# Optimization experiments

Hardware: AMD Instinct MI355X
Metric: run time of the kernel (lower is better)

The kernel has to match this reference:

```python
import jax, jax.numpy as jnp
import numpy as np
import math

HIDDEN = 1024
HEADS = 16
D_K = HIDDEN // HEADS
D_FF = 4 * HIDDEN
EPS = 1e-5


def gelu_tanh(x):
    # exact match of the module's hand-written GELU
    c = math.sqrt(2.0 / math.pi)
    return 0.5 * x * (1.0 + jnp.tanh(c * (x + 0.044715 * x ** 3)))


def layer_norm(x, gamma, beta):
    mu = jnp.mean(x, axis=-1, keepdims=True)
    var = jnp.mean((x - mu) ** 2, axis=-1, keepdims=True)
    return (x - mu) * jax.lax.rsqrt(var + EPS) * gamma + beta


def setup_inputs() -> dict:
    key = jax.random.key(0)
    ks = jax.random.split(key, 16)
    s = 0.02
    B, S, H = 4, 2048, HIDDEN
    return {
        "x": jax.random.normal(ks[0], (B, S, H), dtype=jnp.float32),
        "Wq": jax.random.normal(ks[1], (H, H), dtype=jnp.float32) * s,
        "bq": jnp.zeros((H,), jnp.float32),
        "Wk": jax.random.normal(ks[2], (H, H), dtype=jnp.float32) * s,
        "bk": jnp.zeros((H,), jnp.float32),
        "Wv": jax.random.normal(ks[3], (H, H), dtype=jnp.float32) * s,
        "bv": jnp.zeros((H,), jnp.float32),
        "Wo": jax.random.normal(ks[4], (H, H), dtype=jnp.float32) * s,
        "bo": jnp.zeros((H,), jnp.float32),
        "W1": jax.random.normal(ks[5], (H, D_FF), dtype=jnp.float32) * s,
        "b1": jnp.zeros((D_FF,), jnp.float32),
        "W2": jax.random.normal(ks[6], (D_FF, H), dtype=jnp.float32) * s,
        "b2": jnp.zeros((H,), jnp.float32),
        "g1": jnp.ones((H,), jnp.float32),
        "be1": jnp.zeros((H,), jnp.float32),
        "g2": jnp.ones((H,), jnp.float32),
        "be2": jnp.zeros((H,), jnp.float32),
    }


def reference(x, Wq, bq, Wk, bk, Wv, bv, Wo, bo, W1, b1, W2, b2, g1, be1, g2, be2):
    B, S, H = x.shape
    # QKV projections -> [B, heads, S, d_k]
    def split_heads(t):
        return t.reshape(B, S, HEADS, D_K).transpose(0, 2, 1, 3)
    q = split_heads(x @ Wq + bq)
    k = split_heads(x @ Wk + bk)
    v = split_heads(x @ Wv + bv)
    scores = jnp.einsum("bhsd,bhtd->bhst", q, k) / math.sqrt(D_K)
    attn = jax.nn.softmax(scores, axis=-1)
    ctx = jnp.einsum("bhst,bhtd->bhsd", attn, v)
    ctx = ctx.transpose(0, 2, 1, 3).reshape(B, S, H)
    attn_out = ctx @ Wo + bo
    x = layer_norm(x + attn_out, g1, be1)
    ff = gelu_tanh(x @ W1 + b1) @ W2 + b2
    x = layer_norm(x + ff, g2, be2)
    return x
```

## Files before the change

### kernel.cpp

```cpp
#include <hip/hip_runtime.h>
#include <hip/hip_bf16.h>
#include <math.h>

#define HIDDEN 1024
#define NHEADS 16
#define DK 64
#define DFF 4096
#define SEQ 2048
#define NBATCH 4
#define NTOK (NBATCH*SEQ)

typedef __attribute__((ext_vector_type(8))) short bf16x8;
typedef __attribute__((ext_vector_type(4))) float f32x4;
typedef __attribute__((ext_vector_type(16))) float f32x16;
typedef __attribute__((ext_vector_type(4))) unsigned short us4;
typedef __attribute__((ext_vector_type(2))) unsigned int u32x2;

typedef __attribute__((address_space(1))) void gvoid;
typedef __attribute__((address_space(3))) void lvoid;

__device__ __forceinline__ unsigned short f2b(float f) {
  union { float f; unsigned int u; } v; v.f = f;
  unsigned int u = v.u;
  return (unsigned short)((u + 0x7fffu + ((u >> 16) & 1u)) >> 16);
}

__device__ __forceinline__ unsigned pack_bf16(float lo, float hi) {
  float2 f2; f2.x = lo; f2.y = hi;
  __hip_bfloat162 h = __float22bfloat162_rn(f2);
  union { __hip_bfloat162 h; unsigned u; } c; c.h = h;
  return c.u;
}

__device__ __forceinline__ void gload_lds16(const void* g, void* l) {
  __builtin_amdgcn_global_load_lds((gvoid*)g, (lvoid*)l, 16, 0, 0);
}

__global__ void k_cvt(const float* __restrict__ in, unsigned short* __restrict__ out, int n4) {
  int i = blockIdx.x * blockDim.x + threadIdx.x;
  int stride = gridDim.x * blockDim.x;
  for (; i < n4; i += stride) {
    float4 v = ((const float4*)in)[i];
    us4 o;
    o.x = f2b(v.x); o.y = f2b(v.y); o.z = f2b(v.z); o.w = f2b(v.w);
    ((us4*)out)[i] = o;
  }
}

__global__ void k_transcvt(const float* __restrict__ W, unsigned short* __restrict__ WT,
                           int K, int N, float scale) {
  __shared__ unsigned short tile[64][80];
  int t = threadIdx.x;
  int k0 = blockIdx.x * 64, n0 = blockIdx.y * 64;
  int lr = t >> 2, c0 = (t & 3) * 16;
  const float* src = W + (size_t)(k0 + lr) * N + n0 + c0;
  #pragma unroll
  for (int j = 0; j < 16; ++j) tile[lr][c0 + j] = f2b(src[j] * scale);
  __syncthreads();
  unsigned short* dst = WT + (size_t)(n0 + lr) * K + k0 + c0;
  #pragma unroll
  for (int j = 0; j < 16; ++j) dst[j] = tile[c0 + j][lr];
}

__global__ void k_vtrans(const unsigned short* __restrict__ V, unsigned short* __restrict__ VT) {
  __shared__ unsigned short tile[64][80];
  int bid = blockIdx.x;
  int st = bid & 31, bh = bid >> 5;
  int s0 = st * 64;
  int t = threadIdx.x;
  int lr = t >> 2, c0 = (t & 3) * 16;
  const unsigned short* src = V + (size_t)bh * SEQ * DK + (size_t)(s0 + lr) * DK + c0;
  #pragma unroll
  for (int j = 0; j < 16; ++j) tile[lr][c0 + j] = src[j];
  __syncthreads();
  unsigned short* dst = VT + (size_t)bh * DK * SEQ + (size_t)lr * SEQ + s0 + c0;
  #pragma unroll
  for (int j = 0; j < 16; ++j) dst[j] = tile[c0 + j][lr];
}

template <int MODE>
__global__ __launch_bounds__(256)
void k_gemm(const unsigned short* __restrict__ A, const unsigned short* __restrict__ Bt,
            const float* __restrict__ bias, void* __restrict__ Cout,
            int M, int N, int K, float bscale) {
  __shared__ __align__(1024) char lds[32768];
  const int tid = threadIdx.x;
  const int lane = tid & 63;
  const int wid = tid >> 6;
  const int wm = wid >> 1, wn = wid & 1;
  const int l15 = lane & 15, lg = lane >> 4;
  const int bm = blockIdx.x, bn = blockIdx.y;

  f32x4 acc[4][4] = {};

  const char* Ab = (const char*)A + (size_t)bm * 128 * (size_t)K * 2;
  const char* Bb = (const char*)Bt + (size_t)bn * 128 * (size_t)K * 2;
  const size_t ldr = (size_t)K * 2;

  for (int k0 = 0; k0 < K; k0 += 64) {
    #pragma unroll
    for (int r = 0; r < 4; ++r) {
      int li = tid * 16 + r * 4096;
      int row = li >> 7;
      int col = (li & 127) ^ ((row & 7) << 4);
      gload_lds16(Ab + (size_t)row * ldr + k0 * 2 + col, lds + li);
      gload_lds16(Bb + (size_t)row * ldr + k0 * 2 + col, lds + 16384 + li);
    }
    __syncthreads();
    #pragma unroll
    for (int kc = 0; kc < 2; ++kc) {
      bf16x8 af[4], bfr[4];
      #pragma unroll
      for (int i = 0; i < 4; ++i) {
        int kb = kc * 64 + (lg << 4);
        int lr = wm * 64 + i * 16 + l15;
        af[i] = *(const bf16x8*)(lds + lr * 128 + (kb ^ ((lr & 7) << 4)));
        int lr2 = wn * 64 + i * 16 + l15;
        bfr[i] = *(const bf16x8*)(lds + 16384 + lr2 * 128 + (kb ^ ((lr2 & 7) << 4)));
      }
      #pragma unroll
      for (int mi = 0; mi < 4; ++mi)
        #pragma unroll
        for (int ni = 0; ni < 4; ++ni)
          acc[mi][ni] = __builtin_amdgcn_mfma_f32_16x16x32_bf16(af[mi], bfr[ni], acc[mi][ni], 0, 0, 0);
    }
    __syncthreads();
  }

  const int mbase = bm * 128 + wm * 64;
  const int nbase = bn * 128 + wn * 64;
  #pragma unroll
  for (int ni = 0; ni < 4; ++ni) {
    int n = nbase + ni * 16 + l15;
    float bv = bias[n] * bscale;
    #pragma unroll
    for (int mi = 0; mi < 4; ++mi) {
      #pragma unroll
      for (int r = 0; r < 4; ++r) {
        int m = mbase + mi * 16 + lg * 4 + r;
        float val = acc[mi][ni][r] + bv;
        if (MODE == 0) {
          int b = m >> 11, s = m & 2047;
          int h = n >> 6, d = n & 63;
          ((unsigned short*)Cout)[((size_t)(b * NHEADS + h) * SEQ + s) * DK + d] = f2b(val);
        } else if (MODE == 1) {
          ((float*)Cout)[(size_t)m * N + n] = val;
        } else {
          float x = val;
          float t = tanhf(0.7978845608028654f * (x + 0.044715f * x * x * x));
          ((unsigned short*)Cout)[(size_t)m * N + n] = f2b(0.5f * x * (1.0f + t));
        }
      }
    }
  }
}

__global__ __launch_bounds__(256)
void k_attn(const unsigned short* __restrict__ Qp, const unsigned short* __restrict__ Kp,
            const unsigned short* __restrict__ VTp, unsigned short* __restrict__ ctx) {
  const int tid = threadIdx.x, w = tid >> 6, lane = tid & 63;
  const int l31 = lane & 31, hi = lane >> 5;
  const int bid = blockIdx.x;
  const int qb = bid & 15, bh = bid >> 4;
  const size_t base = (size_t)bh * SEQ * DK;
  const size_t baseT = (size_t)bh * DK * SEQ;
  const int q0 = qb * 128 + w * 32;

  const float L2E = 1.4426950408889634f;
  const float THR = 11.541560327111708f;

  bf16x8 qf[4];
  #pragma unroll
  for (int sl = 0; sl < 4; ++sl)
    qf[sl] = *(const bf16x8*)(Qp + base + (size_t)(q0 + l31) * DK + sl * 16 + hi * 8);

  bf16x8 kf[4];
  #pragma unroll
  for (int sl = 0; sl < 4; ++sl)
    kf[sl] = *(const bf16x8*)(Kp + base + (size_t)l31 * DK + sl * 16 + hi * 8);

  float M = -1e30f, l_run = 0.f;
  f32x16 o0 = {}, o1 = {};

  for (int kv0 = 0; kv0 < SEQ; kv0 += 32) {
    f32x16 s = {};
    __builtin_amdgcn_s_setprio(1);
    #pragma unroll
    for (int sl = 0; sl < 4; ++sl)
      s = __builtin_amdgcn_mfma_f32_32x32x16_bf16(kf[sl], qf[sl], s, 0, 0, 0);
    __builtin_amdgcn_s_setprio(0);

    int kvn = kv0 + 32;
    if (kvn < SEQ) {
      #pragma unroll
      for (int sl = 0; sl < 4; ++sl)
        kf[sl] = *(const bf16x8*)(Kp + base + (size_t)(kvn + l31) * DK + sl * 16 + hi * 8);
    }
    bf16x8 vf00 = *(const bf16x8*)(VTp + baseT + (size_t)(l31) * SEQ + kv0 + hi * 8);
    bf16x8 vf01 = *(const bf16x8*)(VTp + baseT + (size_t)(l31) * SEQ + kv0 + 16 + hi * 8);
    bf16x8 vf10 = *(const bf16x8*)(VTp + baseT + (size_t)(32 + l31) * SEQ + kv0 + hi * 8);
    bf16x8 vf11 = *(const bf16x8*)(VTp + baseT + (size_t)(32 + l31) * SEQ + kv0 + 16 + hi * 8);

    float mx = fmaxf(s[0], s[1]);
    #pragma unroll
    for (int r = 2; r < 16; ++r) mx = fmaxf(mx, s[r]);
    mx = fmaxf(mx, __shfl_xor(mx, 32));
    float mxl = mx * L2E;
    if (!__all(mxl <= M + THR)) {
      float Mnew = fmaxf(M, mxl);
      float corr = __builtin_amdgcn_exp2f(M - Mnew);
      l_run *= corr;
      #pragma unroll
      for (int r = 0; r < 16; ++r) { o0[r] *= corr; o1[r] *= corr; }
      M = Mnew;
    }
    float p[16];
    float sum = 0.f;
    #pragma unroll
    for (int r = 0; r < 16; ++r) {
      p[r] = __builtin_amdgcn_exp2f(fmaf(s[r], L2E, -M));
      sum += p[r];
    }
    sum += __shfl_xor(sum, 32);
    l_run += sum;

    unsigned wds[8];
    #pragma unroll
    for (int g = 0; g < 2; ++g) {
      unsigned w0 = pack_bf16(p[g*8+0], p[g*8+1]);
      unsigned w1 = pack_bf16(p[g*8+2], p[g*8+3]);
      unsigned w2 = pack_bf16(p[g*8+4], p[g*8+5]);
      unsigned w3 = pack_bf16(p[g*8+6], p[g*8+7]);
#if __has_builtin(__builtin_amdgcn_permlane32_swap)
      u32x2 r02 = __builtin_amdgcn_permlane32_swap(w0, w2, false, false);
      u32x2 r13 = __builtin_amdgcn_permlane32_swap(w1, w3, false, false);
      wds[g*4+0] = r02.x; wds[g*4+1] = r13.x;
      wds[g*4+2] = r02.y; wds[g*4+3] = r13.y;
#else
      unsigned s0 = __shfl_xor(w0, 32), s1 = __shfl_xor(w1, 32);
      unsigned s2 = __shfl_xor(w2, 32), s3 = __shfl_xor(w3, 32);
      wds[g*4+0] = hi ? s2 : w0; wds[g*4+1] = hi ? s3 : w1;
      wds[g*4+2] = hi ? w2 : s0; wds[g*4+3] = hi ? w3 : s1;
#endif
    }
    union { unsigned u[4]; bf16x8 v; } pb0, pb1;
    pb0.u[0]=wds[0]; pb0.u[1]=wds[1]; pb0.u[2]=wds[2]; pb0.u[3]=wds[3];
    pb1.u[0]=wds[4]; pb1.u[1]=wds[5]; pb1.u[2]=wds[6]; pb1.u[3]=wds[7];

    __builtin_amdgcn_s_setprio(1);
    o0 = __builtin_amdgcn_mfma_f32_32x32x16_bf16(vf00, pb0.v, o0, 0, 0, 0);
    o1 = __builtin_amdgcn_mfma_f32_32x32x16_bf16(vf10, pb0.v, o1, 0, 0, 0);
    o0 = __builtin_amdgcn_mfma_f32_32x32x16_bf16(vf01, pb1.v, o0, 0, 0, 0);
    o1 = __builtin_amdgcn_mfma_f32_32x32x16_bf16(vf11, pb1.v, o1, 0, 0, 0);
    __builtin_amdgcn_s_setprio(0);
  }

  float inv = 1.f / l_run;
  const int b = bh >> 4, h = bh & 15;
  const int q = q0 + l31;
  size_t rowbase = ((size_t)(b * SEQ + q)) * HIDDEN + h * 64;
  #pragma unroll
  for (int g = 0; g < 4; ++g) {
    us4 st0, st1;
    st0.x = f2b(o0[4*g+0] * inv); st0.y = f2b(o0[4*g+1] * inv);
    st0.z = f2b(o0[4*g+2] * inv); st0.w = f2b(o0[4*g+3] * inv);
    st1.x = f2b(o1[4*g+0] * inv); st1.y = f2b(o1[4*g+1] * inv);
    st1.z = f2b(o1[4*g+2] * inv); st1.w = f2b(o1[4*g+3] * inv);
    int d0 = g * 8 + hi * 4;
    *(us4*)(ctx + rowbase + d0)      = st0;
    *(us4*)(ctx + rowbase + 32 + d0) = st1;
  }
}

__global__ __launch_bounds__(256)
void k_ln(const float* __restrict__ a, const float* __restrict__ b,
          const float* __restrict__ gamma, const float* __restrict__ beta,
          float* __restrict__ outf, unsigned short* __restrict__ outb) {
  int row = blockIdx.x;
  int tid = threadIdx.x;
  const float4* A = (const float4*)(a + (size_t)row * HIDDEN);
  const float4* B = (const float4*)(b + (size_t)row * HIDDEN);
  float4 va = A[tid], vb = B[tid];
  float x0 = va.x + vb.x, x1 = va.y + vb.y, x2 = va.z + vb.z, x3 = va.w + vb.w;
  float sum = x0 + x1 + x2 + x3;
  float sq = x0 * x0 + x1 * x1 + x2 * x2 + x3 * x3;
  #pragma unroll
  for (int d = 1; d < 64; d <<= 1) { sum += __shfl_xor(sum, d); sq += __shfl_xor(sq, d); }
  __shared__ float red[8];
  if ((tid & 63) == 0) { red[(tid >> 6) * 2] = sum; red[(tid >> 6) * 2 + 1] = sq; }
  __syncthreads();
  sum = red[0] + red[2] + red[4] + red[6];
  sq  = red[1] + red[3] + red[5] + red[7];
  float mu = sum * (1.f / HIDDEN);
  float var = sq * (1.f / HIDDEN) - mu * mu;
  float rs = rsqrtf(var + 1e-5f);
  float4 g = ((const float4*)gamma)[tid];
  float4 be = ((const float4*)beta)[tid];
  float y0 = (x0 - mu) * rs * g.x + be.x;
  float y1 = (x1 - mu) * rs * g.y + be.y;
  float y2 = (x2 - mu) * rs * g.z + be.z;
  float y3 = (x3 - mu) * rs * g.w + be.w;
  if (outf) { float4 o; o.x = y0; o.y = y1; o.z = y2; o.w = y3; ((float4*)(outf + (size_t)row * HIDDEN))[tid] = o; }
  if (outb) { us4 o; o.x = f2b(y0); o.y = f2b(y1); o.z = f2b(y2); o.w = f2b(y3); ((us4*)(outb + (size_t)row * HIDDEN))[tid] = o; }
}

#define OFF_XB   ((size_t)0)
#define OFF_WQT  ((size_t)16777216)
#define OFF_WKT  ((size_t)18874368)
#define OFF_WVT  ((size_t)20971520)
#define OFF_WOT  ((size_t)23068672)
#define OFF_W1T  ((size_t)25165824)
#define OFF_W2T  ((size_t)33554432)
#define OFF_Q    ((size_t)41943040)
#define OFF_K    ((size_t)58720256)
#define OFF_V    ((size_t)75497472)
#define OFF_VT   ((size_t)92274688)
#define OFF_AO   ((size_t)109051904)
#define OFF_LN1F ((size_t)142606336)

extern "C" void kernel_launch(void* const* d_in, const int* in_sizes, int n_in,
                              void* d_out, int out_size, void* d_ws, size_t ws_size,
                              hipStream_t stream) {
  const float* x   = (const float*)d_in[0];
  const float* Wq  = (const float*)d_in[1];
  const float* bq  = (const float*)d_in[2];
  const float* Wk  = (const float*)d_in[3];
  const float* bk  = (const float*)d_in[4];
  const float* Wv  = (const float*)d_in[5];
  const float* bv  = (const float*)d_in[6];
  const float* Wo  = (const float*)d_in[7];
  const float* bo  = (const float*)d_in[8];
  const float* W1  = (const float*)d_in[9];
  const float* b1  = (const float*)d_in[10];
  const float* W2  = (const float*)d_in[11];
  const float* b2  = (const float*)d_in[12];
  const float* g1  = (const float*)d_in[13];
  const float* be1 = (const float*)d_in[14];
  const float* g2  = (const float*)d_in[15];
  const float* be2 = (const float*)d_in[16];

  char* ws = (char*)d_ws;
  unsigned short* xb   = (unsigned short*)(ws + OFF_XB);
  unsigned short* wqT  = (unsigned short*)(ws + OFF_WQT);
  unsigned short* wkT  = (unsigned short*)(ws + OFF_WKT);
  unsigned short* wvT  = (unsigned short*)(ws + OFF_WVT);
  unsigned short* woT  = (unsigned short*)(ws + OFF_WOT);
  unsigned short* w1T  = (unsigned short*)(ws + OFF_W1T);
  unsigned short* w2T  = (unsigned short*)(ws + OFF_W2T);
  unsigned short* Qb   = (unsigned short*)(ws + OFF_Q);
  unsigned short* Kb   = (unsigned short*)(ws + OFF_K);
  unsigned short* Vb   = (unsigned short*)(ws + OFF_V);
  unsigned short* VTb  = (unsigned short*)(ws + OFF_VT);
  unsigned short* ctx  = (unsigned short*)(ws + OFF_V);
  float*          ao   = (float*)(ws + OFF_AO);
  float*          ln1f = (float*)(ws + OFF_LN1F);
  unsigned short* ln1b = (unsigned short*)(ws + OFF_XB);
  unsigned short* ff1  = (unsigned short*)(ws + OFF_Q);
  float*          ff2  = (float*)(ws + OFF_AO);

  k_cvt<<<2048, 256, 0, stream>>>(x, xb, NTOK * HIDDEN / 4);

  k_transcvt<<<dim3(16, 16), 256, 0, stream>>>(Wq, wqT, 1024, 1024, 0.125f);
  k_transcvt<<<dim3(16, 16), 256, 0, stream>>>(Wk, wkT, 1024, 1024, 1.0f);
  k_transcvt<<<dim3(16, 16), 256, 0, stream>>>(Wv, wvT, 1024, 1024, 1.0f);
  k_transcvt<<<dim3(16, 16), 256, 0, stream>>>(Wo, woT, 1024, 1024, 1.0f);
  k_transcvt<<<dim3(16, 64), 256, 0, stream>>>(W1, w1T, 1024, 4096, 1.0f);
  k_transcvt<<<dim3(64, 16), 256, 0, stream>>>(W2, w2T, 4096, 1024, 1.0f);

  k_gemm<0><<<dim3(64, 8), 256, 0, stream>>>(xb, wqT, bq, Qb, NTOK, HIDDEN, HIDDEN, 0.125f);
  k_gemm<0><<<dim3(64, 8), 256, 0, stream>>>(xb, wkT, bk, Kb, NTOK, HIDDEN, HIDDEN, 1.0f);
  k_gemm<0><<<dim3(64, 8), 256, 0, stream>>>(xb, wvT, bv, Vb, NTOK, HIDDEN, HIDDEN, 1.0f);

  k_vtrans<<<2048, 256, 0, stream>>>(Vb, VTb);

  k_attn<<<1024, 256, 0, stream>>>(Qb, Kb, VTb, ctx);

  k_gemm<1><<<dim3(64, 8), 256, 0, stream>>>(ctx, woT, bo, ao, NTOK, HIDDEN, HIDDEN, 1.0f);

  k_ln<<<NTOK, 256, 0, stream>>>(x, ao, g1, be1, ln1f, ln1b);

  k_gemm<2><<<dim3(64, 32), 256, 0, stream>>>(ln1b, w1T, b1, ff1, NTOK, DFF, HIDDEN, 1.0f);

  k_gemm<1><<<dim3(64, 8), 256, 0, stream>>>(ff1, w2T, b2, ff2, NTOK, HIDDEN, DFF, 1.0f);

  k_ln<<<NTOK, 256, 0, stream>>>(ln1f, ff2, g2, be2, (float*)d_out, nullptr);
}
```

Measured before the change: 752.9 us.

## Split attention KV range across two blocks and merge partials in combine kernel

The attention kernel now splits each query tile's KV sequence into two halves handled by separate blocks, doubling the grid from 1024 to 2048 blocks. Each block writes unnormalized fp32 partial outputs plus running sum and max, and a new combine kernel rescales and merges them into the bf16 context. It also drops the lazy-rescale threshold and the setprio hints, so the correction multiply now runs every iteration. The aim is more parallelism and occupancy across CUs, at the cost of extra fp32 partial traffic (about 64MB written and read), an extra launch, and more per-iteration rescale work.

```diff
diff --git a/kernel.cpp b/kernel.cpp
--- a/kernel.cpp
+++ b/kernel.cpp
@@ -157,17 +157,20 @@
 
 __global__ __launch_bounds__(256)
 void k_attn(const unsigned short* __restrict__ Qp, const unsigned short* __restrict__ Kp,
-            const unsigned short* __restrict__ VTp, unsigned short* __restrict__ ctx) {
+            const unsigned short* __restrict__ VTp, float* __restrict__ opart,
+            float* __restrict__ lm) {
   const int tid = threadIdx.x, w = tid >> 6, lane = tid & 63;
   const int l31 = lane & 31, hi = lane >> 5;
   const int bid = blockIdx.x;
-  const int qb = bid & 15, bh = bid >> 4;
+  const int half = bid >> 10, inner = bid & 1023;
+  const int qb = inner & 15, bh = inner >> 4;
+  const int tile = inner * 4 + w;
   const size_t base = (size_t)bh * SEQ * DK;
   const size_t baseT = (size_t)bh * DK * SEQ;
   const int q0 = qb * 128 + w * 32;
+  const int kvbeg = half * (SEQ / 2), kvend = kvbeg + SEQ / 2;
 
   const float L2E = 1.4426950408889634f;
-  const float THR = 11.541560327111708f;
 
   bf16x8 qf[4];
   #pragma unroll
@@ -177,21 +180,19 @@
   bf16x8 kf[4];
   #pragma unroll
   for (int sl = 0; sl < 4; ++sl)
-    kf[sl] = *(const bf16x8*)(Kp + base + (size_t)l31 * DK + sl * 16 + hi * 8);
+    kf[sl] = *(const bf16x8*)(Kp + base + (size_t)(kvbeg + l31) * DK + sl * 16 + hi * 8);
 
   float M = -1e30f, l_run = 0.f;
   f32x16 o0 = {}, o1 = {};
 
-  for (int kv0 = 0; kv0 < SEQ; kv0 += 32) {
+  for (int kv0 = kvbeg; kv0 < kvend; kv0 += 32) {
     f32x16 s = {};
-    __builtin_amdgcn_s_setprio(1);
     #pragma unroll
     for (int sl = 0; sl < 4; ++sl)
       s = __builtin_amdgcn_mfma_f32_32x32x16_bf16(kf[sl], qf[sl], s, 0, 0, 0);
-    __builtin_amdgcn_s_setprio(0);
 
     int kvn = kv0 + 32;
-    if (kvn < SEQ) {
+    if (kvn < kvend) {
       #pragma unroll
       for (int sl = 0; sl < 4; ++sl)
         kf[sl] = *(const bf16x8*)(Kp + base + (size_t)(kvn + l31) * DK + sl * 16 + hi * 8);
@@ -205,15 +206,12 @@
     #pragma unroll
     for (int r = 2; r < 16; ++r) mx = fmaxf(mx, s[r]);
     mx = fmaxf(mx, __shfl_xor(mx, 32));
-    float mxl = mx * L2E;
-    if (!__all(mxl <= M + THR)) {
-      float Mnew = fmaxf(M, mxl);
-      float corr = __builtin_amdgcn_exp2f(M - Mnew);
-      l_run *= corr;
-      #pragma unroll
-      for (int r = 0; r < 16; ++r) { o0[r] *= corr; o1[r] *= corr; }
-      M = Mnew;
-    }
+    float Mnew = fmaxf(M, mx * L2E);
+    float corr = __builtin_amdgcn_exp2f(M - Mnew);
+    M = Mnew;
+    l_run *= corr;
+    #pragma unroll
+    for (int r = 0; r < 16; ++r) { o0[r] *= corr; o1[r] *= corr; }
     float p[16];
     float sum = 0.f;
     #pragma unroll
@@ -247,29 +245,57 @@
     pb0.u[0]=wds[0]; pb0.u[1]=wds[1]; pb0.u[2]=wds[2]; pb0.u[3]=wds[3];
     pb1.u[0]=wds[4]; pb1.u[1]=wds[5]; pb1.u[2]=wds[6]; pb1.u[3]=wds[7];
 
-    __builtin_amdgcn_s_setprio(1);
     o0 = __builtin_amdgcn_mfma_f32_32x32x16_bf16(vf00, pb0.v, o0, 0, 0, 0);
     o1 = __builtin_amdgcn_mfma_f32_32x32x16_bf16(vf10, pb0.v, o1, 0, 0, 0);
     o0 = __builtin_amdgcn_mfma_f32_32x32x16_bf16(vf01, pb1.v, o0, 0, 0, 0);
     o1 = __builtin_amdgcn_mfma_f32_32x32x16_bf16(vf11, pb1.v, o1, 0, 0, 0);
-    __builtin_amdgcn_s_setprio(0);
-  }
-
-  float inv = 1.f / l_run;
+  }
+
+  float* op = opart + ((size_t)(half * 4096 + tile)) * 2048 + l31 * 64;
+  #pragma unroll
+  for (int g = 0; g < 4; ++g) {
+    float4 v0; v0.x = o0[4*g+0]; v0.y = o0[4*g+1]; v0.z = o0[4*g+2]; v0.w = o0[4*g+3];
+    float4 v1; v1.x = o1[4*g+0]; v1.y = o1[4*g+1]; v1.z = o1[4*g+2]; v1.w = o1[4*g+3];
+    *(float4*)(op + g * 8 + hi * 4)      = v0;
+    *(float4*)(op + 32 + g * 8 + hi * 4) = v1;
+  }
+  if (hi == 0) {
+    float2 v; v.x = l_run; v.y = M;
+    *(float2*)(lm + ((size_t)(half * 4096 + tile) * 32 + l31) * 2) = v;
+  }
+}
+
+__global__ __launch_bounds__(256)
+void k_comb(const float* __restrict__ opart, const float* __restrict__ lm,
+            unsigned short* __restrict__ ctx) {
+  const int tile = blockIdx.x, t = threadIdx.x;
+  const int q = t >> 3, d0 = (t & 7) * 8;
+  const float* p0 = opart + (size_t)tile * 2048 + q * 64 + d0;
+  const float* p1 = opart + (size_t)(4096 + tile) * 2048 + q * 64 + d0;
+  float2 lm0 = *(const float2*)(lm + ((size_t)tile * 32 + q) * 2);
+  float2 lm1 = *(const float2*)(lm + ((size_t)(4096 + tile) * 32 + q) * 2);
+  float M = fmaxf(lm0.y, lm1.y);
+  float s0 = __builtin_amdgcn_exp2f(lm0.y - M);
+  float s1 = __builtin_amdgcn_exp2f(lm1.y - M);
+  float inv = 1.f / (s0 * lm0.x + s1 * lm1.x);
+  float4 a0 = *(const float4*)p0, a1 = *(const float4*)(p0 + 4);
+  float4 b0 = *(const float4*)p1, b1 = *(const float4*)(p1 + 4);
+  const int w = tile & 3, inner = tile >> 2;
+  const int qb = inner & 15, bh = inner >> 4;
   const int b = bh >> 4, h = bh & 15;
-  const int q = q0 + l31;
-  size_t rowbase = ((size_t)(b * SEQ + q)) * HIDDEN + h * 64;
-  #pragma unroll
-  for (int g = 0; g < 4; ++g) {
-    us4 st0, st1;
-    st0.x = f2b(o0[4*g+0] * inv); st0.y = f2b(o0[4*g+1] * inv);
-    st0.z = f2b(o0[4*g+2] * inv); st0.w = f2b(o0[4*g+3] * inv);
-    st1.x = f2b(o1[4*g+0] * inv); st1.y = f2b(o1[4*g+1] * inv);
-    st1.z = f2b(o1[4*g+2] * inv); st1.w = f2b(o1[4*g+3] * inv);
-    int d0 = g * 8 + hi * 4;
-    *(us4*)(ctx + rowbase + d0)      = st0;
-    *(us4*)(ctx + rowbase + 32 + d0) = st1;
-  }
+  const int stok = qb * 128 + w * 32 + q;
+  size_t o = ((size_t)(b * SEQ + stok)) * HIDDEN + h * 64 + d0;
+  us4 r0, r1;
+  r0.x = f2b((s0 * a0.x + s1 * b0.x) * inv);
+  r0.y = f2b((s0 * a0.y + s1 * b0.y) * inv);
+  r0.z = f2b((s0 * a0.z + s1 * b0.z) * inv);
+  r0.w = f2b((s0 * a0.w + s1 * b0.w) * inv);
+  r1.x = f2b((s0 * a1.x + s1 * b1.x) * inv);
+  r1.y = f2b((s0 * a1.y + s1 * b1.y) * inv);
+  r1.z = f2b((s0 * a1.z + s1 * b1.z) * inv);
+  r1.w = f2b((s0 * a1.w + s1 * b1.w) * inv);
+  *(us4*)(ctx + o)     = r0;
+  *(us4*)(ctx + o + 4) = r1;
 }
 
 __global__ __launch_bounds__(256)
@@ -352,6 +378,8 @@
   unsigned short* Vb   = (unsigned short*)(ws + OFF_V);
   unsigned short* VTb  = (unsigned short*)(ws + OFF_VT);
   unsigned short* ctx  = (unsigned short*)(ws + OFF_V);
+  float*          opart= (float*)(ws + OFF_AO);
+  float*          lmbuf= (float*)(ws + OFF_XB);
   float*          ao   = (float*)(ws + OFF_AO);
   float*          ln1f = (float*)(ws + OFF_LN1F);
   unsigned short* ln1b = (unsigned short*)(ws + OFF_XB);
@@ -373,7 +401,8 @@
 
   k_vtrans<<<2048, 256, 0, stream>>>(Vb, VTb);
 
-  k_attn<<<1024, 256, 0, stream>>>(Qb, Kb, VTb, ctx);
+  k_attn<<<2048, 256, 0, stream>>>(Qb, Kb, VTb, opart, lmbuf);
+  k_comb<<<4096, 256, 0, stream>>>(opart, lmbuf, ctx);
 
   k_gemm<1><<<dim3(64, 8), 256, 0, stream>>>(ctx, woT, bo, ao, NTOK, HIDDEN, HIDDEN, 1.0f);
 
```

After: 718.0 us. 4.6% less time.
